# Kernel tuning notes

Hardware: AMD Instinct MI355X
Metric: run time of the kernel (lower is better)

The kernel has to match this reference:

```python
import jax, jax.numpy as jnp
import numpy as np
from jax import lax

MAX_MEMORY_LR = 0.2
MIN_MEMORY_DECAY = 0.5
MEMORY_MAX_NORM = 15.0
NORM_EPS = 1e-6

def _inv_sig(x):
    x = max(min(x, 0.999), 0.001)
    return float(np.log(x / (1 - x)))

def setup_inputs() -> dict:
    key = jax.random.key(0)
    k1, k2 = jax.random.split(key)
    B, S, D = 16, 4096, 256
    x = jax.random.normal(k1, (B, S, D), dtype=jnp.float32)
    # xavier_uniform with gain=0.1 on (d_out, d_in)
    limit = 0.1 * float(np.sqrt(6.0 / (D + D)))
    M_init = jax.random.uniform(k2, (D, D), dtype=jnp.float32, minval=-limit, maxval=limit)
    eta_raw = jnp.asarray(_inv_sig(0.05), dtype=jnp.float32)
    alpha_raw = jnp.asarray(_inv_sig(0.9), dtype=jnp.float32)
    return {"x": x, "M_init": M_init, "eta_raw": eta_raw, "alpha_raw": alpha_raw}

def reference(x, M_init, eta_raw, alpha_raw):
    # x: [B, S, d_in], M_init: [d_out, d_in]
    B = x.shape[0]
    eta = jax.nn.sigmoid(eta_raw) * MAX_MEMORY_LR
    alpha = MIN_MEMORY_DECAY + jax.nn.sigmoid(alpha_raw) * (1.0 - MIN_MEMORY_DECAY)
    M0 = jnp.broadcast_to(M_init, (B,) + M_init.shape)

    def step(M, x_t):  # M: [B, d_out, d_in], x_t: [B, d_in]
        out_t = jnp.einsum('boi,bi->bo', M, x_t)  # retrieve
        # key = F.normalize(x_t): x / max(||x||, eps)
        k = x_t / jnp.maximum(jnp.linalg.norm(x_t, axis=-1, keepdims=True), NORM_EPS)
        Mk = jnp.einsum('boi,bi->bo', M, k)
        err = out_t - Mk  # value is out_t (self-generated)
        M_new = alpha * M + eta * err[:, :, None] * k[:, None, :]  # rank-1 delta update
        fro = jnp.sqrt(jnp.sum(M_new * M_new, axis=(-2, -1), keepdims=True))
        scale = jnp.minimum(MEMORY_MAX_NORM / (fro + 1e-6), 1.0)
        return M_new * scale, out_t

    M_final, outs = lax.scan(step, M0, jnp.swapaxes(x, 0, 1))
    return jnp.swapaxes(outs, 0, 1), M_final
```

## Files before the change

### kernel.cpp

```cpp
#include <hip/hip_runtime.h>
#include <hip/hip_bf16.h>
#include <math.h>

typedef float  f32x4  __attribute__((ext_vector_type(4)));
typedef short  bf16x4 __attribute__((ext_vector_type(4)));
typedef __bf16 bfv4   __attribute__((ext_vector_type(4)));

#define B_    16
#define S_    4096
#define D_    256
#define CK_   16
#define NC_   (S_ / CK_)
#define NP_   (NC_ / 2)
#define PBLOB_ 1664
#define W_    4

__device__ __forceinline__ f32x4 mfma_bf16(bf16x4 a, bf16x4 b, f32x4 c) {
#if defined(__has_builtin) && __has_builtin(__builtin_amdgcn_mfma_f32_16x16x16bf16_1k)
    return __builtin_amdgcn_mfma_f32_16x16x16bf16_1k(a, b, c, 0, 0, 0);
#else
    f32x4 d;
    asm("v_mfma_f32_16x16x16_bf16 %0, %1, %2, %3" : "=v"(d) : "v"(a), "v"(b), "v"(c));
    return d;
#endif
}
__device__ __forceinline__ bf16x4 pk4(f32x4 v) {
    bfv4 h;
    h[0] = (__bf16)v[0]; h[1] = (__bf16)v[1]; h[2] = (__bf16)v[2]; h[3] = (__bf16)v[3];
    return __builtin_bit_cast(bf16x4, h);
}
__device__ __forceinline__ f32x4 up4(bf16x4 h) {
    f32x4 r;
    r[0] = __uint_as_float(((unsigned)(unsigned short)h[0]) << 16);
    r[1] = __uint_as_float(((unsigned)(unsigned short)h[1]) << 16);
    r[2] = __uint_as_float(((unsigned)(unsigned short)h[2]) << 16);
    r[3] = __uint_as_float(((unsigned)(unsigned short)h[3]) << 16);
    return r;
}

__global__ __launch_bounds__(64) void ldm_prep(
    const float* __restrict__ x,
    const float* __restrict__ eta_raw,
    const float* __restrict__ alpha_raw,
    unsigned char* __restrict__ blob)
{
    const int lane = threadIdx.x;
    const int b = blockIdx.x & 15;
    const int p = blockIdx.x >> 4;
    const int l15 = lane & 15;
    const int q   = lane >> 4;

    __shared__ float Ga[256], Gb[256], Gxs[256];
    __shared__ float csh[32];
    __shared__ float Ts[2][256];

    const float* xa = x + ((size_t)b * S_ + (size_t)p * 32 + l15) * D_ + q * 4;
    const float* xc = xa + 16 * D_;

    const f32x4 z = {0,0,0,0};
    f32x4 ga1=z, ga2=z, ga3=z, gb1=z, gb2=z, gb3=z, gx1=z, gx2=z, gx3=z;
    #pragma unroll 4
    for (int kb = 0; kb < 16; ++kb) {
        f32x4 va = *(const f32x4*)(xa + kb * 16);
        f32x4 vb = *(const f32x4*)(xc + kb * 16);
        bf16x4 ha = pk4(va), la = pk4(va - up4(ha));
        bf16x4 hb = pk4(vb), lb = pk4(vb - up4(hb));
        ga1 = mfma_bf16(ha, ha, ga1);
        ga2 = mfma_bf16(ha, la, ga2);
        ga3 = mfma_bf16(la, ha, ga3);
        gb1 = mfma_bf16(hb, hb, gb1);
        gb2 = mfma_bf16(hb, lb, gb2);
        gb3 = mfma_bf16(lb, hb, gb3);
        gx1 = mfma_bf16(hb, ha, gx1);
        gx2 = mfma_bf16(hb, la, gx2);
        gx3 = mfma_bf16(lb, ha, gx3);
    }
    f32x4 ga = (ga1 + ga2) + ga3;
    f32x4 gb = (gb1 + gb2) + gb3;
    f32x4 gx = (gx1 + gx2) + gx3;
    *(f32x4*)(&Ga[l15 * 16 + q * 4]) = ga;
    *(f32x4*)(&Gb[l15 * 16 + q * 4]) = gb;
    #pragma unroll
    for (int r = 0; r < 4; ++r) Gxs[(q * 4 + r) * 16 + l15] = gx[r];
    __syncthreads();

    const float eta   = 0.2f / (1.0f + expf(-eta_raw[0]));
    const float alpha = 0.5f + 0.5f / (1.0f + expf(-alpha_raw[0]));
    if (lane < 32) {
        const float* G = (lane < 16) ? Ga : Gb;
        float gtt = G[l15 * 17];
        float n   = fmaxf(sqrtf(gtt), 1e-6f);
        float inv = 1.0f / n;
        csh[lane] = eta * (1.0f - inv) * inv / alpha;
    }
    __syncthreads();

    if (lane < 32) {
        const int j = l15;
        const float* G  = (lane < 16) ? Ga : Gb;
        const float* cp = (lane < 16) ? csh : csh + 16;
        float cr[16];
        #pragma unroll
        for (int k = 0; k < 16; ++k) cr[k] = cp[k];
        float Tcol[16];
        Tcol[0] = 0.f;
        #pragma unroll
        for (int t = 1; t < 16; ++t) {
            float acc = cr[j] * G[t * 16 + j];
            #pragma unroll
            for (int k = 1; k < 15; ++k)
                if (k < t) acc += cr[k] * G[t * 16 + k] * Tcol[k];
            Tcol[t] = (t > j) ? acc : 0.f;
        }
        float* Tsj = Ts[lane >> 4];
        #pragma unroll
        for (int t = 0; t < 16; ++t) Tsj[t * 16 + j] = Tcol[t];
    }
    __syncthreads();

    unsigned char* bp = blob + (size_t)(b * NP_ + p) * PBLOB_;
    const int idx = l15 * 16 + q * 4;
    *(bf16x4*)(bp + idx * 2)        = pk4(*(const f32x4*)(&Ts[0][idx]));
    *(bf16x4*)(bp + 512 + idx * 2)  = pk4(*(const f32x4*)(&Ts[1][idx]));
    *(bf16x4*)(bp + 1024 + idx * 2) = pk4(*(const f32x4*)(&Gxs[idx]));
    if (lane < 32) ((float*)(bp + 1536))[lane] = csh[lane];
}

__global__ __launch_bounds__(256, 1) void ldm_main(
    const float* __restrict__ x,
    const float* __restrict__ Minit,
    const float* __restrict__ alpha_raw,
    const unsigned char* __restrict__ blob,
    float* __restrict__ out)
{
    const int tid    = threadIdx.x;
    const int lane   = tid & 63;
    const int w      = __builtin_amdgcn_readfirstlane(tid >> 6);
    const int batch  = blockIdx.x & 15;
    const int rowblk = blockIdx.x >> 4;
    const int l15    = lane & 15;
    const int q      = lane >> 4;
    const int col0   = w * 64;

    __shared__ f32x4 parts[2][W_][2][64];

    const float alpha = 0.5f + 0.5f / (1.0f + expf(-alpha_raw[0]));
    const float a2 = alpha * alpha, a4 = a2 * a2, a8 = a4 * a4, a16 = a8 * a8;
    const float a32 = a16 * a16;
    const float aq = (q == 0) ? 1.f : (q == 1) ? a4 : (q == 2) ? a8 : a8 * a4;
    const f32x4 apowA = { aq, aq * alpha, aq * a2, aq * a2 * alpha };
    const f32x4 apowB = apowA * a16;

    const int s = l15 - (q << 2);
    bf16x4 IB;
    IB[0] = (s == 0) ? (short)0x3F80 : (short)0;
    IB[1] = (s == 1) ? (short)0x3F80 : (short)0;
    IB[2] = (s == 2) ? (short)0x3F80 : (short)0;
    IB[3] = (s == 3) ? (short)0x3F80 : (short)0;

    const int mrow = rowblk * 16 + l15;
    f32x4 master[4];
    #pragma unroll
    for (int cb = 0; cb < 4; ++cb)
        master[cb] = *(const f32x4*)(Minit + (size_t)mrow * D_ + col0 + cb * 16 + q * 4);

    const float* xbb = x + (size_t)batch * S_ * D_;
    const unsigned char* bb0 = blob + (size_t)batch * NP_ * PBLOB_;
    const int tfoff = (l15 * 16 + q * 4) * 2;

    const float* xr = xbb + (size_t)l15 * D_ + col0 + q * 4;
    const float* xptr;
    const unsigned char* bptr;
    float* outpj = out + (size_t)batch * S_ * D_ + rowblk * 16 + l15
                 + (size_t)q * 4 * D_;

    struct BlobT { bf16x4 Ta, Tb, Gx; f32x4 ca, cb; };
    BlobT bA, bB;
    bf16x4 XA[8], XB[8];
    f32x4  Xf[8];
    const f32x4 zz = {0,0,0,0};

    {
        #pragma unroll
        for (int cb = 0; cb < 4; ++cb) {
            Xf[cb]     = *(const f32x4*)(xr + cb * 16);
            Xf[4 + cb] = *(const f32x4*)(xr + 16 * D_ + cb * 16);
        }
        #pragma unroll
        for (int i = 0; i < 8; ++i) XA[i] = pk4(Xf[i]);
        bA.Ta = *(const bf16x4*)(bb0 + tfoff);
        bA.Tb = *(const bf16x4*)(bb0 + 512 + tfoff);
        bA.Gx = *(const bf16x4*)(bb0 + 1024 + tfoff);
        bA.ca = *(const f32x4*)(bb0 + 1536 + q * 16);
        bA.cb = *(const f32x4*)(bb0 + 1600 + q * 16);
        xptr = xr + 32 * D_;
        bptr = bb0 + PBLOB_;
    }

    auto body = [&](int j, bf16x4 (&Xc)[8], bf16x4 (&Xn)[8], BlobT& bc, BlobT& bn) {
        const int par = j & 1;
        #pragma unroll
        for (int cb = 0; cb < 4; ++cb) {
            Xf[cb]     = *(const f32x4*)(xptr + cb * 16);
            Xf[4 + cb] = *(const f32x4*)(xptr + 16 * D_ + cb * 16);
        }
        bn.Ta = *(const bf16x4*)(bptr + tfoff);
        bn.Tb = *(const bf16x4*)(bptr + 512 + tfoff);
        bn.Gx = *(const bf16x4*)(bptr + 1024 + tfoff);
        bn.ca = *(const f32x4*)(bptr + 1536 + q * 16);
        bn.cb = *(const f32x4*)(bptr + 1600 + q * 16);
        if (j < NP_ - 2) { xptr += 32 * D_; bptr += PBLOB_; }

        bf16x4 mf[4];
        #pragma unroll
        for (int cb = 0; cb < 4; ++cb) mf[cb] = pk4(master[cb]);
        f32x4 acca = zz, accb = zz;
        #pragma unroll
        for (int cb = 0; cb < 4; ++cb) {
            acca = mfma_bf16(Xc[cb],     mf[cb], acca);
            accb = mfma_bf16(Xc[4 + cb], mf[cb], accb);
        }
        parts[par][w][0][lane] = acca;
        parts[par][w][1][lane] = accb;

        bf16x4 ta[4], tb[4];
        #pragma unroll
        for (int cb = 0; cb < 4; ++cb) {
            ta[cb] = pk4(mfma_bf16(Xc[cb],     IB, zz));
            tb[cb] = pk4(mfma_bf16(Xc[4 + cb], IB, zz));
        }
        __syncthreads();

        f32x4 pa0 = parts[par][0][0][lane], pa1 = parts[par][1][0][lane];
        f32x4 pa2 = parts[par][2][0][lane], pa3 = parts[par][3][0][lane];
        f32x4 pb0 = parts[par][0][1][lane], pb1 = parts[par][1][1][lane];
        f32x4 pb2 = parts[par][2][1][lane], pb3 = parts[par][3][1][lane];
        f32x4 bba = (pa0 + pa1) + (pa2 + pa3);
        f32x4 bbb = (pb0 + pb1) + (pb2 + pb3);

        f32x4 da = mfma_bf16(bc.Ta, pk4(bba), bba);
        if (w == 2) {
            #pragma unroll
            for (int r = 0; r < 4; ++r) outpj[r * D_] = da[r] * apowA[r];
        }
        bf16x4 ea = pk4(da * bc.ca);
        f32x4 bb2 = mfma_bf16(bc.Gx, ea, bbb);
        f32x4 db = mfma_bf16(bc.Tb, pk4(bb2), bb2);
        if (w == 3) {
            #pragma unroll
            for (int r = 0; r < 4; ++r) outpj[(16 + r) * D_] = db[r] * apowB[r];
        }
        bf16x4 eb = pk4(db * bc.cb);

        #pragma unroll
        for (int cb = 0; cb < 4; ++cb) {
            f32x4 m = mfma_bf16(ta[cb], ea, master[cb]);
            master[cb] = mfma_bf16(tb[cb], eb, m) * a32;
        }

        #pragma unroll
        for (int i = 0; i < 8; ++i) Xn[i] = pk4(Xf[i]);
        outpj += 32 * D_;
    };

    for (int j = 0; j < NP_; j += 2) {
        body(j,     XA, XB, bA, bB);
        body(j + 1, XB, XA, bB, bA);
    }

    float* Mout = out + (size_t)B_ * S_ * D_
                + ((size_t)batch * D_ + mrow) * D_;
    #pragma unroll
    for (int cb = 0; cb < 4; ++cb)
        *(f32x4*)(Mout + col0 + cb * 16 + q * 4) = master[cb];
}

extern "C" void kernel_launch(void* const* d_in, const int* in_sizes, int n_in,
                              void* d_out, int out_size, void* d_ws, size_t ws_size,
                              hipStream_t stream) {
    const float* x         = (const float*)d_in[0];
    const float* Minit     = (const float*)d_in[1];
    const float* eta_raw   = (const float*)d_in[2];
    const float* alpha_raw = (const float*)d_in[3];
    float* out = (float*)d_out;
    unsigned char* blob = (unsigned char*)d_ws;

    hipLaunchKernelGGL(ldm_prep, dim3(B_ * NP_), dim3(64), 0, stream,
                       x, eta_raw, alpha_raw, blob);
    hipLaunchKernelGGL(ldm_main, dim3(B_ * 16), dim3(256), 0, stream,
                       x, Minit, alpha_raw, blob, out);
}
```

Before: 271.8 us.

## Precompute bf16 x and its transpose in prep kernel for the sequential main loop

The prep kernel now also writes a bf16 copy of x and a per-chunk transposed bf16 copy into the workspace, producing the transpose through an MFMA against an identity matrix. A new main kernel loads these prepacked operands directly instead of reading fp32 x and converting or transposing it inside the serial recurrence loop. This halves the bytes read in the latency-bound loop and removes the in-loop packing work, at the cost of extra writes in the prep kernel and a large workspace. The old path is kept as a fallback when the workspace is too small.

```diff
diff --git a/kernel.cpp b/kernel.cpp
--- a/kernel.cpp
+++ b/kernel.cpp
@@ -15,6 +15,11 @@
 #define PBLOB_ 1664
 #define W_    4
 
+#define XBF_OFF  ((size_t)4 << 20)
+#define XT_OFF   (XBF_OFF + ((size_t)32 << 20))
+#define WS_BIG_  (XT_OFF + ((size_t)32 << 20))
+#define PAIRB_   16384
+
 __device__ __forceinline__ f32x4 mfma_bf16(bf16x4 a, bf16x4 b, f32x4 c) {
 #if defined(__has_builtin) && __has_builtin(__builtin_amdgcn_mfma_f32_16x16x16bf16_1k)
     return __builtin_amdgcn_mfma_f32_16x16x16bf16_1k(a, b, c, 0, 0, 0);
@@ -42,7 +47,8 @@
     const float* __restrict__ x,
     const float* __restrict__ eta_raw,
     const float* __restrict__ alpha_raw,
-    unsigned char* __restrict__ blob)
+    unsigned char* __restrict__ ws,
+    int big)
 {
     const int lane = threadIdx.x;
     const int b = blockIdx.x & 15;
@@ -56,6 +62,16 @@
 
     const float* xa = x + ((size_t)b * S_ + (size_t)p * 32 + l15) * D_ + q * 4;
     const float* xc = xa + 16 * D_;
+
+    const int s = l15 - (q << 2);
+    bf16x4 IB;
+    IB[0] = (s == 0) ? (short)0x3F80 : (short)0;
+    IB[1] = (s == 1) ? (short)0x3F80 : (short)0;
+    IB[2] = (s == 2) ? (short)0x3F80 : (short)0;
+    IB[3] = (s == 3) ? (short)0x3F80 : (short)0;
+
+    unsigned char* xbf_p = ws + XBF_OFF + ((size_t)(b * NP_ + p)) * PAIRB_;
+    unsigned char* xt_p  = ws + XT_OFF  + ((size_t)(b * NP_ + p)) * PAIRB_;
 
     const f32x4 z = {0,0,0,0};
     f32x4 ga1=z, ga2=z, ga3=z, gb1=z, gb2=z, gb3=z, gx1=z, gx2=z, gx3=z;
@@ -74,6 +90,14 @@
         gx1 = mfma_bf16(hb, ha, gx1);
         gx2 = mfma_bf16(hb, la, gx2);
         gx3 = mfma_bf16(lb, ha, gx3);
+        if (big) {
+            *(bf16x4*)(xbf_p + ((size_t)(l15 * 256 + kb * 16 + q * 4)) * 2) = ha;
+            *(bf16x4*)(xbf_p + ((size_t)((16 + l15) * 256 + kb * 16 + q * 4)) * 2) = hb;
+            f32x4 txa = mfma_bf16(ha, IB, z);
+            f32x4 txb = mfma_bf16(hb, IB, z);
+            *(bf16x4*)(xt_p + ((size_t)((kb * 16 + l15) * 32 + q * 4)) * 2)      = pk4(txa);
+            *(bf16x4*)(xt_p + ((size_t)((kb * 16 + l15) * 32 + 16 + q * 4)) * 2) = pk4(txb);
+        }
     }
     f32x4 ga = (ga1 + ga2) + ga3;
     f32x4 gb = (gb1 + gb2) + gb3;
@@ -118,7 +142,7 @@
     }
     __syncthreads();
 
-    unsigned char* bp = blob + (size_t)(b * NP_ + p) * PBLOB_;
+    unsigned char* bp = ws + (size_t)(b * NP_ + p) * PBLOB_;
     const int idx = l15 * 16 + q * 4;
     *(bf16x4*)(bp + idx * 2)        = pk4(*(const f32x4*)(&Ts[0][idx]));
     *(bf16x4*)(bp + 512 + idx * 2)  = pk4(*(const f32x4*)(&Ts[1][idx]));
@@ -126,11 +150,11 @@
     if (lane < 32) ((float*)(bp + 1536))[lane] = csh[lane];
 }
 
-__global__ __launch_bounds__(256, 1) void ldm_main(
+__global__ __launch_bounds__(256, 1) void ldm_main_small(
     const float* __restrict__ x,
     const float* __restrict__ Minit,
     const float* __restrict__ alpha_raw,
-    const unsigned char* __restrict__ blob,
+    const unsigned char* __restrict__ ws,
     float* __restrict__ out)
 {
     const int tid    = threadIdx.x;
@@ -165,7 +189,7 @@
         master[cb] = *(const f32x4*)(Minit + (size_t)mrow * D_ + col0 + cb * 16 + q * 4);
 
     const float* xbb = x + (size_t)batch * S_ * D_;
-    const unsigned char* bb0 = blob + (size_t)batch * NP_ * PBLOB_;
+    const unsigned char* bb0 = ws + (size_t)batch * NP_ * PBLOB_;
     const int tfoff = (l15 * 16 + q * 4) * 2;
 
     const float* xr = xbb + (size_t)l15 * D_ + col0 + q * 4;
@@ -275,6 +299,142 @@
         *(f32x4*)(Mout + col0 + cb * 16 + q * 4) = master[cb];
 }
 
+__global__ __launch_bounds__(256, 1) void ldm_main_big(
+    const float* __restrict__ Minit,
+    const float* __restrict__ alpha_raw,
+    const unsigned char* __restrict__ ws,
+    float* __restrict__ out)
+{
+    const int tid    = threadIdx.x;
+    const int lane   = tid & 63;
+    const int w      = __builtin_amdgcn_readfirstlane(tid >> 6);
+    const int batch  = blockIdx.x & 15;
+    const int rowblk = blockIdx.x >> 4;
+    const int l15    = lane & 15;
+    const int q      = lane >> 4;
+    const int col0   = w * 64;
+
+    __shared__ f32x4 parts[2][W_][2][64];
+
+    const float alpha = 0.5f + 0.5f / (1.0f + expf(-alpha_raw[0]));
+    const float a2 = alpha * alpha, a4 = a2 * a2, a8 = a4 * a4, a16 = a8 * a8;
+    const float a32 = a16 * a16;
+    const float aq = (q == 0) ? 1.f : (q == 1) ? a4 : (q == 2) ? a8 : a8 * a4;
+    const f32x4 apowA = { aq, aq * alpha, aq * a2, aq * a2 * alpha };
+    const f32x4 apowB = apowA * a16;
+
+    const int mrow = rowblk * 16 + l15;
+    f32x4 master[4];
+    #pragma unroll
+    for (int cb = 0; cb < 4; ++cb)
+        master[cb] = *(const f32x4*)(Minit + (size_t)mrow * D_ + col0 + cb * 16 + q * 4);
+
+    const unsigned char* bb0 = ws + (size_t)batch * NP_ * PBLOB_;
+    const int tfoff = (l15 * 16 + q * 4) * 2;
+
+    const unsigned char* xbf = ws + XBF_OFF + (size_t)batch * NP_ * PAIRB_
+                             + ((size_t)(l15 * 256 + col0 + q * 4)) * 2;
+    const unsigned char* xt  = ws + XT_OFF  + (size_t)batch * NP_ * PAIRB_
+                             + ((size_t)((col0 + l15) * 32 + q * 4)) * 2;
+    float* outpj = out + (size_t)batch * S_ * D_ + rowblk * 16 + l15
+                 + (size_t)q * 4 * D_;
+
+    struct BlobT { bf16x4 Ta, Tb, Gx; f32x4 ca, cb; };
+    BlobT bA, bB;
+    bf16x4 XA[8], XB[8];
+    bf16x4 taA[4], tbA[4], taB[4], tbB[4];
+    const f32x4 zz = {0,0,0,0};
+
+    {
+        #pragma unroll
+        for (int cb = 0; cb < 4; ++cb) {
+            XA[cb]     = *(const bf16x4*)(xbf + cb * 32);
+            XA[4 + cb] = *(const bf16x4*)(xbf + 8192 + cb * 32);
+            taA[cb]    = *(const bf16x4*)(xt + cb * 1024);
+            tbA[cb]    = *(const bf16x4*)(xt + cb * 1024 + 32);
+        }
+        bA.Ta = *(const bf16x4*)(bb0 + tfoff);
+        bA.Tb = *(const bf16x4*)(bb0 + 512 + tfoff);
+        bA.Gx = *(const bf16x4*)(bb0 + 1024 + tfoff);
+        bA.ca = *(const f32x4*)(bb0 + 1536 + q * 16);
+        bA.cb = *(const f32x4*)(bb0 + 1600 + q * 16);
+    }
+    const unsigned char* xnptr = xbf + PAIRB_;
+    const unsigned char* xtptr = xt + PAIRB_;
+    const unsigned char* bptr  = bb0 + PBLOB_;
+
+    auto body = [&](int j, bf16x4 (&Xc)[8], bf16x4 (&Xn)[8],
+                    bf16x4 (&tac)[4], bf16x4 (&tbc)[4],
+                    bf16x4 (&tan)[4], bf16x4 (&tbn)[4], BlobT& bc, BlobT& bn) {
+        const int par = j & 1;
+        #pragma unroll
+        for (int cb = 0; cb < 4; ++cb) {
+            Xn[cb]     = *(const bf16x4*)(xnptr + cb * 32);
+            Xn[4 + cb] = *(const bf16x4*)(xnptr + 8192 + cb * 32);
+            tan[cb]    = *(const bf16x4*)(xtptr + cb * 1024);
+            tbn[cb]    = *(const bf16x4*)(xtptr + cb * 1024 + 32);
+        }
+        bn.Ta = *(const bf16x4*)(bptr + tfoff);
+        bn.Tb = *(const bf16x4*)(bptr + 512 + tfoff);
+        bn.Gx = *(const bf16x4*)(bptr + 1024 + tfoff);
+        bn.ca = *(const f32x4*)(bptr + 1536 + q * 16);
+        bn.cb = *(const f32x4*)(bptr + 1600 + q * 16);
+        if (j < NP_ - 2) { xnptr += PAIRB_; xtptr += PAIRB_; bptr += PBLOB_; }
+
+        bf16x4 mf[4];
+        #pragma unroll
+        for (int cb = 0; cb < 4; ++cb) mf[cb] = pk4(master[cb]);
+        f32x4 acca = zz, accb = zz;
+        #pragma unroll
+        for (int cb = 0; cb < 4; ++cb) {
+            acca = mfma_bf16(Xc[cb],     mf[cb], acca);
+            accb = mfma_bf16(Xc[4 + cb], mf[cb], accb);
+        }
+        parts[par][w][0][lane] = acca;
+        parts[par][w][1][lane] = accb;
+        __syncthreads();
+
+        f32x4 pa0 = parts[par][0][0][lane], pa1 = parts[par][1][0][lane];
+        f32x4 pa2 = parts[par][2][0][lane], pa3 = parts[par][3][0][lane];
+        f32x4 pb0 = parts[par][0][1][lane], pb1 = parts[par][1][1][lane];
+        f32x4 pb2 = parts[par][2][1][lane], pb3 = parts[par][3][1][lane];
+        f32x4 bba = (pa0 + pa1) + (pa2 + pa3);
+        f32x4 bbb = (pb0 + pb1) + (pb2 + pb3);
+
+        f32x4 da = mfma_bf16(bc.Ta, pk4(bba), bba);
+        if (w == 2) {
+            #pragma unroll
+            for (int r = 0; r < 4; ++r) outpj[r * D_] = da[r] * apowA[r];
+        }
+        bf16x4 ea = pk4(da * bc.ca);
+        f32x4 bb2 = mfma_bf16(bc.Gx, ea, bbb);
+        f32x4 db = mfma_bf16(bc.Tb, pk4(bb2), bb2);
+        if (w == 3) {
+            #pragma unroll
+            for (int r = 0; r < 4; ++r) outpj[(16 + r) * D_] = db[r] * apowB[r];
+        }
+        bf16x4 eb = pk4(db * bc.cb);
+
+        #pragma unroll
+        for (int cb = 0; cb < 4; ++cb) {
+            f32x4 m = mfma_bf16(tac[cb], ea, master[cb]);
+            master[cb] = mfma_bf16(tbc[cb], eb, m) * a32;
+        }
+        outpj += 32 * D_;
+    };
+
+    for (int j = 0; j < NP_; j += 2) {
+        body(j,     XA, XB, taA, tbA, taB, tbB, bA, bB);
+        body(j + 1, XB, XA, taB, tbB, taA, tbA, bB, bA);
+    }
+
+    float* Mout = out + (size_t)B_ * S_ * D_
+                + ((size_t)batch * D_ + mrow) * D_;
+    #pragma unroll
+    for (int cb = 0; cb < 4; ++cb)
+        *(f32x4*)(Mout + col0 + cb * 16 + q * 4) = master[cb];
+}
+
 extern "C" void kernel_launch(void* const* d_in, const int* in_sizes, int n_in,
                               void* d_out, int out_size, void* d_ws, size_t ws_size,
                               hipStream_t stream) {
@@ -283,10 +443,17 @@
     const float* eta_raw   = (const float*)d_in[2];
     const float* alpha_raw = (const float*)d_in[3];
     float* out = (float*)d_out;
-    unsigned char* blob = (unsigned char*)d_ws;
+    unsigned char* ws = (unsigned char*)d_ws;
+
+    const int big = (ws_size >= WS_BIG_) ? 1 : 0;
 
     hipLaunchKernelGGL(ldm_prep, dim3(B_ * NP_), dim3(64), 0, stream,
-                       x, eta_raw, alpha_raw, blob);
-    hipLaunchKernelGGL(ldm_main, dim3(B_ * 16), dim3(256), 0, stream,
-                       x, Minit, alpha_raw, blob, out);
-}
+                       x, eta_raw, alpha_raw, ws, big);
+    if (big) {
+        hipLaunchKernelGGL(ldm_main_big, dim3(B_ * 16), dim3(256), 0, stream,
+                           Minit, alpha_raw, ws, out);
+    } else {
+        hipLaunchKernelGGL(ldm_main_small, dim3(B_ * 16), dim3(256), 0, stream,
+                           x, Minit, alpha_raw, ws, out);
+    }
+}
```

Result: slower. 331.3 us (+21.9%).
